# Kernel tuning notes

Measured on AMD Instinct MI355X. Metric: run time of the kernel, lower is better.

Reference implementation:

```python
import jax, jax.numpy as jnp
import numpy as np

PAD, BOS, EOS, UNK = 0, 1, 2, 3
B, S, V, D, L = 256, 512, 50000, 256, 128

def setup_inputs() -> dict:
    key = jax.random.key(0)
    ks = jax.random.split(key, 12)
    vocab_tensor = jax.random.randint(ks[0], (B, S), 4, V)
    parent_idx = jax.random.randint(ks[1], (B, S), 0, S)
    pbond = jax.random.randint(ks[2], (B, S), 0, 4)
    bond = jax.random.randint(ks[3], (B, S), 0, 4)
    patom = jax.random.randint(ks[4], (B, S), 0, 16)
    atom = jax.random.randint(ks[5], (B, S), 0, 16)
    btype = jax.random.randint(ks[6], (B, S), 0, 4)
    order_tensor = jnp.stack([parent_idx, pbond, bond, patom, atom, btype], axis=-1)
    lengths = jax.random.randint(ks[7], (B,), 1, S + 1)
    mask_tensor = jnp.arange(S)[None, :] < lengths[:, None]  # ragged prefix masks
    eps = jax.random.normal(ks[8], (B, L), dtype=jnp.float32)
    sc = 1.0 / np.sqrt(D)
    emb = jax.random.normal(ks[9], (V, D), dtype=jnp.float32) * sc
    Wm = jax.random.normal(ks[10], (D, L), dtype=jnp.float32) * sc
    Wv = jax.random.normal(ks[11], (D, L), dtype=jnp.float32) * sc
    Wlin = jax.random.normal(jax.random.fold_in(key, 20), (L, D), dtype=jnp.float32) / np.sqrt(L)
    Wout = jax.random.normal(jax.random.fold_in(key, 21), (D, D), dtype=jnp.float32) * sc
    return {
        'vocab_tensor': vocab_tensor, 'order_tensor': order_tensor, 'mask_tensor': mask_tensor,
        'eps': eps, 'emb': emb, 'Wm': Wm, 'bm': jnp.zeros((L,), jnp.float32),
        'Wv': Wv, 'bv': jnp.zeros((L,), jnp.float32), 'Wlin': Wlin,
        'blin': jnp.zeros((D,), jnp.float32), 'Wout': Wout, 'bout': jnp.zeros((D,), jnp.float32),
    }

def _forward(vocab_tensor, order_tensor, mask_tensor, eps, emb, Wm, bm, Wv, bv, Wlin, blin, Wout, bout):
    # --- mask bond-pos columns (torch.where assignments, vectorized) ---
    # (columns 1 and 2 set to -1 where masked; kept implicitly via vt/pad handling)
    # --- calc_chem_z path: masked vocab, parent gather, edge one-hot ---
    vt = jnp.where(mask_tensor, vocab_tensor, PAD)                      # [B,S]
    vocab_emb = emb[vt]                                                 # [B,S,D]
    oi = order_tensor[..., 0]
    oi = jnp.where(oi == -1, BOS, oi)
    parent = jnp.where(mask_tensor, jnp.take_along_axis(vt, oi, axis=1), PAD)
    parent = parent.at[:, 0].set(BOS)
    parent_emb = emb[parent]                                            # [B,S,D]
    idx = jnp.clip(order_tensor[..., 5] - 1, -1, None)
    edge_type = jnp.where((idx >= 0)[..., None],
                          jax.nn.one_hot(jnp.clip(idx, 0), 3, dtype=jnp.float32), 0.0)  # [B,S,3]
    # pooling stand-in for (undefined) StructureEncoder -> [B,D]
    m = mask_tensor[..., None].astype(jnp.float32)
    enc = ((vocab_emb + parent_emb) * m).sum(1) / jnp.maximum(m.sum(1), 1.0)
    enc = enc * (1.0 + 0.0 * edge_type.sum())  # keep edge_type in graph
    # --- LatentSampler ---
    mean = enc @ Wm + bm
    log_var = enc @ Wv + bv
    z = mean + eps * jnp.exp(0.5 * log_var)
    memory = z @ Wlin + blin                                            # [B,D]
    # --- vectorized bos/eos/pad sequence assembly (the hot loop in torch) ---
    inp = jnp.concatenate([jnp.full((B, 1), BOS, vocab_tensor.dtype), vocab_tensor], axis=1)  # [B,S+1]
    mask_ex = jnp.concatenate([jnp.ones((B, 1), bool), mask_tensor], axis=1)
    tgt = jnp.roll(inp, -1, axis=1)
    first_false = jnp.argmax(~mask_ex, axis=1)                          # first eos position
    has_false = jnp.any(~mask_ex, axis=1)
    pos = jnp.arange(S + 1)[None, :]
    tgt = jnp.where(has_false[:, None] & (pos == first_false[:, None] - 1), EOS, tgt)
    kill = has_false[:, None] & (pos >= first_false[:, None])
    tgt = jnp.where(kill, PAD, tgt)
    inp = jnp.where(kill, PAD, inp)
    # edge_index assembly (faithful, consumed by decoder in original)
    padneg = jnp.full((B, 1), -1, order_tensor.dtype)
    edge_index = jnp.concatenate([padneg, jnp.where(mask_tensor, order_tensor[..., 0], -2) + 1], axis=1)
    # --- embedding lookups + decoder stand-in + output head ---
    node_embed = emb[inp]                                               # [B,S+1,D]
    dec = node_embed + memory[:, None, :]
    dec = dec + 0.0 * edge_index[..., None].astype(jnp.float32)         # keep edge_index in graph
    word_emb = dec @ Wout + bout
    tgt_emb = emb[tgt]
    valid = (tgt != PAD)
    sq = (word_emb - tgt_emb) ** 2 * valid[..., None]
    token_loss = sq.sum() / jnp.maximum(valid.sum() * D, 1).astype(jnp.float32)
    kl = -0.5 * jnp.sum(1.0 + log_var - mean ** 2 - jnp.exp(log_var)) / B
    return token_loss, kl

def reference(vocab_tensor, order_tensor, mask_tensor, eps, emb, Wm, bm, Wv, bv, Wlin, blin, Wout, bout):
    return _forward(vocab_tensor, order_tensor, mask_tensor, eps, emb, Wm, bm, Wv, bv, Wlin, blin, Wout, bout)
```

## Files before the change

kernel.cpp:

```cpp
#include <hip/hip_runtime.h>

#define B_ 256
#define S_ 512
#define V_ 50000
#define D_ 256
#define L_ 128
#define NGB 768
#define NENC 256
#define NCH (V_ / 16)
#define NSPLIT 8
#define K2B (B_ * NSPLIT)

typedef __attribute__((ext_vector_type(8))) short short8;
typedef __attribute__((ext_vector_type(4))) float floatx4;

#define OFF_SQP 16
#define OFF_KL  (OFF_SQP + K2B)
#define OFF_CNT (OFF_KL + 256)
#define OFF_Q   (OFF_CNT + 256)
#define OFF_P   (OFF_Q + B_ * D_)
#define OFF_EB  (OFF_P + V_ * D_ / 2)
#define OFF_WB  (OFF_EB + V_ * D_ / 2)

__device__ __forceinline__ unsigned short f2bf(float x) {
    unsigned u = __float_as_uint(x);
    u += 0x7FFFu + ((u >> 16) & 1u);
    return (unsigned short)(u >> 16);
}
__device__ __forceinline__ float bf2f(unsigned short u) {
    return __uint_as_float(((unsigned)u) << 16);
}

__global__ __launch_bounds__(256) void prep0(const float* __restrict__ Wout,
                                             float* __restrict__ ws) {
    unsigned short* __restrict__ Wb = (unsigned short*)(ws + OFF_WB);
    const int t = blockIdx.x * 256 + threadIdx.x;
    const int idx0 = t * 4;
    const int kk = idx0 >> 13;
    const int col = (idx0 >> 5) & 255;
    const int hi = (idx0 >> 3) & 3;
    const int e0 = idx0 & 7;
    const int kbase = kk * 32 + hi * 8 + e0;
    ushort4 h;
    h.x = f2bf(Wout[(size_t)(kbase + 0) * D_ + col]);
    h.y = f2bf(Wout[(size_t)(kbase + 1) * D_ + col]);
    h.z = f2bf(Wout[(size_t)(kbase + 2) * D_ + col]);
    h.w = f2bf(Wout[(size_t)(kbase + 3) * D_ + col]);
    ((ushort4*)Wb)[t] = h;
}

__global__ __launch_bounds__(256, 2) void fused1(
    const int* __restrict__ vocab, const int* __restrict__ order,
    const int* __restrict__ mask, const float* __restrict__ emb,
    const float* __restrict__ eps, const float* __restrict__ Wm,
    const float* __restrict__ bm, const float* __restrict__ Wv,
    const float* __restrict__ bv, const float* __restrict__ Wlin,
    const float* __restrict__ blin, const float* __restrict__ Wout,
    const float* __restrict__ bout, float* __restrict__ ws) {
    __shared__ __align__(16) char smem[16384];
    const int tid = threadIdx.x;

    if (blockIdx.x < NGB) {
        unsigned short* __restrict__ P = (unsigned short*)(ws + OFF_P);
        unsigned short* __restrict__ EB = (unsigned short*)(ws + OFF_EB);
        const unsigned short* __restrict__ Wb = (const unsigned short*)(ws + OFF_WB);
        const int lane = tid & 63, wv = tid >> 6;
        const int lo = lane & 15, hi = lane >> 4;
        short8 bfr[4][8];
#pragma unroll
        for (int nt = 0; nt < 4; ++nt)
#pragma unroll
            for (int kk = 0; kk < 8; ++kk)
                bfr[nt][kk] = *(const short8*)(Wb + kk * 8192 +
                                               (wv * 64 + nt * 16 + lo) * 32 + hi * 8);
        int ch = blockIdx.x;
        float4 R[4];
        {
            const float4* src = (const float4*)emb + (size_t)ch * 1024;
#pragma unroll
            for (int i = 0; i < 4; ++i) R[i] = src[i * 256 + tid];
        }
        for (; ch < NCH; ch += NGB) {
#pragma unroll
            for (int i = 0; i < 4; ++i) {
                const int e = (i * 256 + tid) * 4;
                const int row = e >> 8, colb = (e & 255) * 2;
                const int byt = (row * 512 + colb) ^ ((row & 7) << 4);
                ushort4 h;
                h.x = f2bf(R[i].x); h.y = f2bf(R[i].y);
                h.z = f2bf(R[i].z); h.w = f2bf(R[i].w);
                *(ushort4*)(smem + byt) = h;
            }
            __syncthreads();
            const int chn = ch + NGB;
            float4 Rn[4] = {R[0], R[1], R[2], R[3]};
            if (chn < NCH) {
                const float4* src = (const float4*)emb + (size_t)chn * 1024;
#pragma unroll
                for (int i = 0; i < 4; ++i) Rn[i] = src[i * 256 + tid];
            }
            floatx4 acc[4];
#pragma unroll
            for (int nt = 0; nt < 4; ++nt) acc[nt] = (floatx4){0.f, 0.f, 0.f, 0.f};
#pragma unroll
            for (int kk = 0; kk < 8; ++kk) {
                const int byt = (lo * 512 + hi * 16 + kk * 64) ^ ((lo & 7) << 4);
                short8 a = *(const short8*)(smem + byt);
#pragma unroll
                for (int nt = 0; nt < 4; ++nt)
                    acc[nt] = __builtin_amdgcn_mfma_f32_16x16x32_bf16(
                        a, bfr[nt][kk], acc[nt], 0, 0, 0);
            }
            {
                const int o0 = tid * 32;
                const int sw = ((o0 >> 9) & 7) << 4;
                ushort4 e0 = *(const ushort4*)(smem + (o0 ^ sw));
                ushort4 e1 = *(const ushort4*)(smem + ((o0 + 16) ^ sw));
                ushort4* dst = (ushort4*)((char*)EB + (size_t)ch * 8192 + o0);
                dst[0] = e0; dst[1] = e1;
            }
#pragma unroll
            for (int r = 0; r < 4; ++r) {
                const int row = hi * 4 + r;
#pragma unroll
                for (int nt = 0; nt < 4; ++nt) {
                    const int col = wv * 64 + nt * 16 + lo;
                    const int off = (row * 512 + col * 2) ^ (((row >> 2) & 3) << 5);
                    *(unsigned short*)(smem + 8192 + off) = f2bf(acc[nt][r]);
                }
            }
            __syncthreads();
            {
                const int o0 = tid * 32;
                const int sw = (((o0 >> 9) >> 2) & 3) << 5;
                ushort4 c0 = *(const ushort4*)(smem + 8192 + (o0 ^ sw));
                ushort4 c1 = *(const ushort4*)(smem + 8192 + ((o0 + 16) ^ sw));
                ushort4* dst = (ushort4*)((char*)P + (size_t)ch * 8192 + o0);
                dst[0] = c0; dst[1] = c1;
            }
#pragma unroll
            for (int i = 0; i < 4; ++i) R[i] = Rn[i];
        }
        return;
    }
    int* s_id1 = (int*)smem;
    int* s_id2 = s_id1 + S_;
    float4* s_part = (float4*)(smem + 4096);
    float* s_enc = (float*)(smem + 7168);
    float* s_mean = (float*)(smem + 8192);
    float* s_lv = (float*)(smem + 8704);
    float* s_z = (float*)(smem + 9216);
    float* s_mem = (float*)(smem + 9728);
    float* s_red = (float*)(smem + 10752);
    int* s_cntp = (int*)(smem + 11776);
    const int b = blockIdx.x - NGB;
    if (tid == 0) *s_cntp = 0;
    __syncthreads();
    for (int j = tid; j < S_; j += 256) {
        const int mk = mask[b * S_ + j];
        int id1 = 0, id2 = 0;
        if (mk) {
            id1 = vocab[b * S_ + j];
            if (j == 0) {
                id2 = 1;
            } else {
                int oi = order[(size_t)(b * S_ + j) * 6];
                if (oi == -1) oi = 1;
                id2 = mask[b * S_ + oi] ? vocab[b * S_ + oi] : 0;
            }
        }
        s_id1[j] = id1;
        s_id2[j] = id2;
        unsigned long long bal = __ballot(mk != 0);
        if ((tid & 63) == 0) atomicAdd(s_cntp, __popcll(bal));
    }
    __syncthreads();
    const int cnt = *s_cntp;
    const int jg = tid >> 6, d4 = tid & 63;
    const float4* eb4 = (const float4*)emb;
    float4 a = {0.f, 0.f, 0.f, 0.f};
#pragma unroll 4
    for (int j = jg; j < cnt; j += 4) {
        float4 x = eb4[(size_t)s_id1[j] * 64 + d4];
        float4 y = eb4[(size_t)s_id2[j] * 64 + d4];
        a.x += x.x + y.x; a.y += x.y + y.y;
        a.z += x.z + y.z; a.w += x.w + y.w;
    }
    if (jg) s_part[(jg - 1) * 64 + d4] = a;
    __syncthreads();
    if (jg == 0) {
#pragma unroll
        for (int g = 0; g < 3; ++g) {
            float4 p = s_part[g * 64 + d4];
            a.x += p.x; a.y += p.y; a.z += p.z; a.w += p.w;
        }
        const float inv = 1.f / fmaxf((float)cnt, 1.f);
        a.x *= inv; a.y *= inv; a.z *= inv; a.w *= inv;
        ((float4*)s_enc)[d4] = a;
    }
    __syncthreads();
    {
        const int l = tid & (L_ - 1);
        const float* W = (tid < L_) ? Wm : Wv;
        const float* bb = (tid < L_) ? bm : bv;
        float dot = bb[l];
        for (int d = 0; d < D_; ++d) dot = fmaf(s_enc[d], W[d * L_ + l], dot);
        if (tid < L_) s_mean[l] = dot; else s_lv[l] = dot;
    }
    __syncthreads();
    float klp = 0.f;
    if (tid < L_) {
        float mn = s_mean[tid], lv = s_lv[tid];
        s_z[tid] = mn + eps[b * L_ + tid] * expf(0.5f * lv);
        klp = 1.f + lv - mn * mn - expf(lv);
    }
    s_red[tid] = klp;
    __syncthreads();
    for (int s = 128; s > 0; s >>= 1) {
        if (tid < s) s_red[tid] += s_red[tid + s];
        __syncthreads();
    }
    if (tid == 0) {
        ws[OFF_KL + b] = s_red[0];
        ((int*)ws)[OFF_CNT + b] = cnt;
    }
    {
        float mem = blin[tid];
        for (int l2 = 0; l2 < L_; ++l2) mem = fmaf(s_z[l2], Wlin[l2 * D_ + tid], mem);
        s_mem[tid] = mem;
    }
    __syncthreads();
    {
        float qv = bout[tid];
        for (int k = 0; k < D_; ++k) qv = fmaf(s_mem[k], Wout[k * D_ + tid], qv);
        ws[OFF_Q + b * D_ + tid] = qv;
    }
}

__global__ __launch_bounds__(256) void scan2(const int* __restrict__ vocab,
                                             float* __restrict__ ws) {
    __shared__ int s_sid[80];
    __shared__ float s_wred[4];
    const int tid = threadIdx.x;
    const int b = blockIdx.x >> 3, part = blockIdx.x & 7;
    const unsigned short* __restrict__ P = (const unsigned short*)(ws + OFF_P);
    const unsigned short* __restrict__ EB = (const unsigned short*)(ws + OFF_EB);
    const int cnt = ((const int*)ws)[OFF_CNT + b];
    const int npos = cnt + 1;
    const int per = (npos + NSPLIT - 1) / NSPLIT;
    const int j0 = part * per;
    const int jend = min(j0 + per, npos);
    const int lo_s = (j0 > 0) ? j0 - 1 : 0;
    const int nstage = min(jend, cnt) - lo_s;
    if (tid < nstage) s_sid[tid] = vocab[b * S_ + lo_s + tid];
    __syncthreads();
    const int jgq = tid >> 6, lane = tid & 63, c = lane * 4;
    const float4 q4 = *(const float4*)(ws + OFF_Q + b * D_ + c);
    float acc = 0.f;
    for (int jj = j0 + jgq * 4; jj < jend; jj += 16) {
        int inp[4], tgt[4];
        float wgt[4];
#pragma unroll
        for (int u = 0; u < 4; ++u) {
            const int j = jj + u;
            const bool v = (j < jend);
            const int jc = v ? j : jj;
            inp[u] = (jc == 0) ? 1 : s_sid[jc - 1 - lo_s];
            tgt[u] = (jc < cnt) ? s_sid[jc - lo_s] : ((cnt < S_) ? 2 : 1);
            wgt[u] = v ? 1.f : 0.f;
        }
        ushort4 pv[4], tv[4];
#pragma unroll
        for (int u = 0; u < 4; ++u) {
            pv[u] = *(const ushort4*)(P + (size_t)inp[u] * D_ + c);
            tv[u] = *(const ushort4*)(EB + (size_t)tgt[u] * D_ + c);
        }
#pragma unroll
        for (int u = 0; u < 4; ++u) {
            float d0 = bf2f(pv[u].x) + q4.x - bf2f(tv[u].x);
            float d1 = bf2f(pv[u].y) + q4.y - bf2f(tv[u].y);
            float d2 = bf2f(pv[u].z) + q4.z - bf2f(tv[u].z);
            float d3 = bf2f(pv[u].w) + q4.w - bf2f(tv[u].w);
            float s = fmaf(d0, d0, fmaf(d1, d1, fmaf(d2, d2, d3 * d3)));
            acc = fmaf(wgt[u], s, acc);
        }
    }
#pragma unroll
    for (int off = 32; off; off >>= 1) acc += __shfl_down(acc, off, 64);
    if (lane == 0) s_wred[jgq] = acc;
    __syncthreads();
    if (tid == 0)
        ws[OFF_SQP + blockIdx.x] = s_wred[0] + s_wred[1] + s_wred[2] + s_wred[3];
}

__global__ __launch_bounds__(256) void finalize3(const float* __restrict__ ws,
                                                 float* __restrict__ out) {
    __shared__ float s_red[256];
    const int tid = threadIdx.x;
    float sq = 0.f;
#pragma unroll
    for (int i = 0; i < NSPLIT; ++i) sq += ws[OFF_SQP + i * 256 + tid];
    s_red[tid] = sq;
    __syncthreads();
    for (int s = 128; s > 0; s >>= 1) {
        if (tid < s) s_red[tid] += s_red[tid + s];
        __syncthreads();
    }
    const float sq_tot = s_red[0];
    __syncthreads();
    s_red[tid] = ws[OFF_KL + tid];
    __syncthreads();
    for (int s = 128; s > 0; s >>= 1) {
        if (tid < s) s_red[tid] += s_red[tid + s];
        __syncthreads();
    }
    const float kl_tot = s_red[0];
    __syncthreads();
    s_red[tid] = (float)(((const int*)ws)[OFF_CNT + tid] + 1);
    __syncthreads();
    for (int s = 128; s > 0; s >>= 1) {
        if (tid < s) s_red[tid] += s_red[tid + s];
        __syncthreads();
    }
    if (tid == 0) {
        float denom = s_red[0] * (float)D_;
        if (denom < 1.f) denom = 1.f;
        out[0] = sq_tot / denom;
        out[1] = -0.5f * kl_tot / (float)B_;
    }
}

extern "C" void kernel_launch(void* const* d_in, const int* in_sizes, int n_in,
                              void* d_out, int out_size, void* d_ws, size_t ws_size,
                              hipStream_t stream) {
    const int* vocab = (const int*)d_in[0];
    const int* order = (const int*)d_in[1];
    const int* mask  = (const int*)d_in[2];
    const float* eps  = (const float*)d_in[3];
    const float* emb  = (const float*)d_in[4];
    const float* Wm   = (const float*)d_in[5];
    const float* bm   = (const float*)d_in[6];
    const float* Wv   = (const float*)d_in[7];
    const float* bv   = (const float*)d_in[8];
    const float* Wlin = (const float*)d_in[9];
    const float* blin = (const float*)d_in[10];
    const float* Wout = (const float*)d_in[11];
    const float* bout = (const float*)d_in[12];

    float* ws = (float*)d_ws;
    prep0<<<64, 256, 0, stream>>>(Wout, ws);
    fused1<<<NGB + NENC, 256, 0, stream>>>(vocab, order, mask, emb, eps, Wm, bm,
                                           Wv, bv, Wlin, blin, Wout, bout, ws);
    scan2<<<K2B, 256, 0, stream>>>(vocab, ws);
    finalize3<<<1, 256, 0, stream>>>(ws, (float*)d_out);
}
```

Measured before the change: 171.1 us.

## Compute projections only for gathered tokens instead of projecting the whole vocabulary

```diff
diff --git a/kernel.cpp b/kernel.cpp
--- a/kernel.cpp
+++ b/kernel.cpp
@@ -5,22 +5,18 @@
 #define V_ 50000
 #define D_ 256
 #define L_ 128
-#define NGB 768
-#define NENC 256
-#define NCH (V_ / 16)
-#define NSPLIT 8
-#define K2B (B_ * NSPLIT)
+#define NPK 64
+#define NSP2 4
+#define NLB (B_ * NSP2)
 
 typedef __attribute__((ext_vector_type(8))) short short8;
 typedef __attribute__((ext_vector_type(4))) float floatx4;
 
 #define OFF_SQP 16
-#define OFF_KL  (OFF_SQP + K2B)
+#define OFF_KL  (OFF_SQP + NLB)
 #define OFF_CNT (OFF_KL + 256)
 #define OFF_Q   (OFF_CNT + 256)
-#define OFF_P   (OFF_Q + B_ * D_)
-#define OFF_EB  (OFF_P + V_ * D_ / 2)
-#define OFF_WB  (OFF_EB + V_ * D_ / 2)
+#define OFF_WB  (OFF_Q + B_ * D_)
 
 __device__ __forceinline__ unsigned short f2bf(float x) {
     unsigned u = __float_as_uint(x);
@@ -31,25 +27,7 @@
     return __uint_as_float(((unsigned)u) << 16);
 }
 
-__global__ __launch_bounds__(256) void prep0(const float* __restrict__ Wout,
-                                             float* __restrict__ ws) {
-    unsigned short* __restrict__ Wb = (unsigned short*)(ws + OFF_WB);
-    const int t = blockIdx.x * 256 + threadIdx.x;
-    const int idx0 = t * 4;
-    const int kk = idx0 >> 13;
-    const int col = (idx0 >> 5) & 255;
-    const int hi = (idx0 >> 3) & 3;
-    const int e0 = idx0 & 7;
-    const int kbase = kk * 32 + hi * 8 + e0;
-    ushort4 h;
-    h.x = f2bf(Wout[(size_t)(kbase + 0) * D_ + col]);
-    h.y = f2bf(Wout[(size_t)(kbase + 1) * D_ + col]);
-    h.z = f2bf(Wout[(size_t)(kbase + 2) * D_ + col]);
-    h.w = f2bf(Wout[(size_t)(kbase + 3) * D_ + col]);
-    ((ushort4*)Wb)[t] = h;
-}
-
-__global__ __launch_bounds__(256, 2) void fused1(
+__global__ __launch_bounds__(256) void enc1(
     const int* __restrict__ vocab, const int* __restrict__ order,
     const int* __restrict__ mask, const float* __restrict__ emb,
     const float* __restrict__ eps, const float* __restrict__ Wm,
@@ -57,90 +35,23 @@
     const float* __restrict__ bv, const float* __restrict__ Wlin,
     const float* __restrict__ blin, const float* __restrict__ Wout,
     const float* __restrict__ bout, float* __restrict__ ws) {
-    __shared__ __align__(16) char smem[16384];
+    __shared__ __align__(16) char smem[11904];
     const int tid = threadIdx.x;
-
-    if (blockIdx.x < NGB) {
-        unsigned short* __restrict__ P = (unsigned short*)(ws + OFF_P);
-        unsigned short* __restrict__ EB = (unsigned short*)(ws + OFF_EB);
-        const unsigned short* __restrict__ Wb = (const unsigned short*)(ws + OFF_WB);
-        const int lane = tid & 63, wv = tid >> 6;
-        const int lo = lane & 15, hi = lane >> 4;
-        short8 bfr[4][8];
-#pragma unroll
-        for (int nt = 0; nt < 4; ++nt)
-#pragma unroll
-            for (int kk = 0; kk < 8; ++kk)
-                bfr[nt][kk] = *(const short8*)(Wb + kk * 8192 +
-                                               (wv * 64 + nt * 16 + lo) * 32 + hi * 8);
-        int ch = blockIdx.x;
-        float4 R[4];
-        {
-            const float4* src = (const float4*)emb + (size_t)ch * 1024;
-#pragma unroll
-            for (int i = 0; i < 4; ++i) R[i] = src[i * 256 + tid];
-        }
-        for (; ch < NCH; ch += NGB) {
-#pragma unroll
-            for (int i = 0; i < 4; ++i) {
-                const int e = (i * 256 + tid) * 4;
-                const int row = e >> 8, colb = (e & 255) * 2;
-                const int byt = (row * 512 + colb) ^ ((row & 7) << 4);
-                ushort4 h;
-                h.x = f2bf(R[i].x); h.y = f2bf(R[i].y);
-                h.z = f2bf(R[i].z); h.w = f2bf(R[i].w);
-                *(ushort4*)(smem + byt) = h;
-            }
-            __syncthreads();
-            const int chn = ch + NGB;
-            float4 Rn[4] = {R[0], R[1], R[2], R[3]};
-            if (chn < NCH) {
-                const float4* src = (const float4*)emb + (size_t)chn * 1024;
-#pragma unroll
-                for (int i = 0; i < 4; ++i) Rn[i] = src[i * 256 + tid];
-            }
-            floatx4 acc[4];
-#pragma unroll
-            for (int nt = 0; nt < 4; ++nt) acc[nt] = (floatx4){0.f, 0.f, 0.f, 0.f};
-#pragma unroll
-            for (int kk = 0; kk < 8; ++kk) {
-                const int byt = (lo * 512 + hi * 16 + kk * 64) ^ ((lo & 7) << 4);
-                short8 a = *(const short8*)(smem + byt);
-#pragma unroll
-                for (int nt = 0; nt < 4; ++nt)
-                    acc[nt] = __builtin_amdgcn_mfma_f32_16x16x32_bf16(
-                        a, bfr[nt][kk], acc[nt], 0, 0, 0);
-            }
-            {
-                const int o0 = tid * 32;
-                const int sw = ((o0 >> 9) & 7) << 4;
-                ushort4 e0 = *(const ushort4*)(smem + (o0 ^ sw));
-                ushort4 e1 = *(const ushort4*)(smem + ((o0 + 16) ^ sw));
-                ushort4* dst = (ushort4*)((char*)EB + (size_t)ch * 8192 + o0);
-                dst[0] = e0; dst[1] = e1;
-            }
-#pragma unroll
-            for (int r = 0; r < 4; ++r) {
-                const int row = hi * 4 + r;
-#pragma unroll
-                for (int nt = 0; nt < 4; ++nt) {
-                    const int col = wv * 64 + nt * 16 + lo;
-                    const int off = (row * 512 + col * 2) ^ (((row >> 2) & 3) << 5);
-                    *(unsigned short*)(smem + 8192 + off) = f2bf(acc[nt][r]);
-                }
-            }
-            __syncthreads();
-            {
-                const int o0 = tid * 32;
-                const int sw = (((o0 >> 9) >> 2) & 3) << 5;
-                ushort4 c0 = *(const ushort4*)(smem + 8192 + (o0 ^ sw));
-                ushort4 c1 = *(const ushort4*)(smem + 8192 + ((o0 + 16) ^ sw));
-                ushort4* dst = (ushort4*)((char*)P + (size_t)ch * 8192 + o0);
-                dst[0] = c0; dst[1] = c1;
-            }
-#pragma unroll
-            for (int i = 0; i < 4; ++i) R[i] = Rn[i];
-        }
+    if (blockIdx.x < NPK) {
+        unsigned short* __restrict__ Wb = (unsigned short*)(ws + OFF_WB);
+        const int t = blockIdx.x * 256 + tid;
+        const int idx0 = t * 4;
+        const int kk = idx0 >> 13;
+        const int col = (idx0 >> 5) & 255;
+        const int hi = (idx0 >> 3) & 3;
+        const int e0 = idx0 & 7;
+        const int kbase = kk * 32 + hi * 8 + e0;
+        ushort4 h;
+        h.x = f2bf(Wout[(size_t)(kbase + 0) * D_ + col]);
+        h.y = f2bf(Wout[(size_t)(kbase + 1) * D_ + col]);
+        h.z = f2bf(Wout[(size_t)(kbase + 2) * D_ + col]);
+        h.w = f2bf(Wout[(size_t)(kbase + 3) * D_ + col]);
+        ((ushort4*)Wb)[t] = h;
         return;
     }
     int* s_id1 = (int*)smem;
@@ -153,7 +64,7 @@
     float* s_mem = (float*)(smem + 9728);
     float* s_red = (float*)(smem + 10752);
     int* s_cntp = (int*)(smem + 11776);
-    const int b = blockIdx.x - NGB;
+    const int b = blockIdx.x - NPK;
     if (tid == 0) *s_cntp = 0;
     __syncthreads();
     for (int j = tid; j < S_; j += 256) {
@@ -237,57 +148,83 @@
     }
 }
 
-__global__ __launch_bounds__(256) void scan2(const int* __restrict__ vocab,
-                                             float* __restrict__ ws) {
-    __shared__ int s_sid[80];
+__global__ __launch_bounds__(256, 2) void loss2(const int* __restrict__ vocab,
+                                                const float* __restrict__ emb,
+                                                float* __restrict__ ws) {
+    __shared__ __align__(16) char smem[8192];
+    __shared__ int s_inp[16], s_tgt[16];
+    __shared__ float s_w[16];
+    __shared__ float s_q[256];
     __shared__ float s_wred[4];
     const int tid = threadIdx.x;
-    const int b = blockIdx.x >> 3, part = blockIdx.x & 7;
-    const unsigned short* __restrict__ P = (const unsigned short*)(ws + OFF_P);
-    const unsigned short* __restrict__ EB = (const unsigned short*)(ws + OFF_EB);
+    const int b = blockIdx.x >> 2, part = blockIdx.x & 3;
+    const int lane = tid & 63, wv = tid >> 6;
+    const int lo = lane & 15, hi = lane >> 4;
+    const unsigned short* __restrict__ Wb = (const unsigned short*)(ws + OFF_WB);
     const int cnt = ((const int*)ws)[OFF_CNT + b];
-    const int npos = cnt + 1;
-    const int per = (npos + NSPLIT - 1) / NSPLIT;
-    const int j0 = part * per;
-    const int jend = min(j0 + per, npos);
-    const int lo_s = (j0 > 0) ? j0 - 1 : 0;
-    const int nstage = min(jend, cnt) - lo_s;
-    if (tid < nstage) s_sid[tid] = vocab[b * S_ + lo_s + tid];
-    __syncthreads();
-    const int jgq = tid >> 6, lane = tid & 63, c = lane * 4;
-    const float4 q4 = *(const float4*)(ws + OFF_Q + b * D_ + c);
-    float acc = 0.f;
-    for (int jj = j0 + jgq * 4; jj < jend; jj += 16) {
-        int inp[4], tgt[4];
-        float wgt[4];
-#pragma unroll
-        for (int u = 0; u < 4; ++u) {
-            const int j = jj + u;
-            const bool v = (j < jend);
-            const int jc = v ? j : jj;
-            inp[u] = (jc == 0) ? 1 : s_sid[jc - 1 - lo_s];
-            tgt[u] = (jc < cnt) ? s_sid[jc - lo_s] : ((cnt < S_) ? 2 : 1);
-            wgt[u] = v ? 1.f : 0.f;
-        }
-        ushort4 pv[4], tv[4];
-#pragma unroll
-        for (int u = 0; u < 4; ++u) {
-            pv[u] = *(const ushort4*)(P + (size_t)inp[u] * D_ + c);
-            tv[u] = *(const ushort4*)(EB + (size_t)tgt[u] * D_ + c);
-        }
-#pragma unroll
-        for (int u = 0; u < 4; ++u) {
-            float d0 = bf2f(pv[u].x) + q4.x - bf2f(tv[u].x);
-            float d1 = bf2f(pv[u].y) + q4.y - bf2f(tv[u].y);
-            float d2 = bf2f(pv[u].z) + q4.z - bf2f(tv[u].z);
-            float d3 = bf2f(pv[u].w) + q4.w - bf2f(tv[u].w);
-            float s = fmaf(d0, d0, fmaf(d1, d1, fmaf(d2, d2, d3 * d3)));
-            acc = fmaf(wgt[u], s, acc);
-        }
-    }
-#pragma unroll
-    for (int off = 32; off; off >>= 1) acc += __shfl_down(acc, off, 64);
-    if (lane == 0) s_wred[jgq] = acc;
+    const int ntiles = (cnt + 16) >> 4;
+    s_q[tid] = ws[OFF_Q + b * D_ + tid];
+    short8 bfr[4][8];
+#pragma unroll
+    for (int nt = 0; nt < 4; ++nt)
+#pragma unroll
+        for (int kk = 0; kk < 8; ++kk)
+            bfr[nt][kk] = *(const short8*)(Wb + kk * 8192 +
+                                           (wv * 64 + nt * 16 + lo) * 32 + hi * 8);
+    float sqacc = 0.f;
+    for (int ti = part; ti < ntiles; ti += NSP2) {
+        if (tid < 16) {
+            const int j = ti * 16 + tid;
+            int inp = 1, tgt = 1;
+            float w = 0.f;
+            if (j <= cnt) {
+                inp = (j == 0) ? 1 : vocab[b * S_ + j - 1];
+                tgt = (j < cnt) ? vocab[b * S_ + j] : ((cnt < S_) ? 2 : 1);
+                w = 1.f;
+            }
+            s_inp[tid] = inp; s_tgt[tid] = tgt; s_w[tid] = w;
+        }
+        __syncthreads();
+#pragma unroll
+        for (int i = 0; i < 4; ++i) {
+            const int fi = i * 256 + tid;
+            const int row = fi >> 6, cf4 = fi & 63;
+            float4 v = *((const float4*)(emb + (size_t)s_inp[row] * D_) + cf4);
+            ushort4 h;
+            h.x = f2bf(v.x); h.y = f2bf(v.y); h.z = f2bf(v.z); h.w = f2bf(v.w);
+            const int byt = (row * 512 + cf4 * 8) ^ ((row & 7) << 4);
+            *(ushort4*)(smem + byt) = h;
+        }
+        __syncthreads();
+        floatx4 acc[4];
+#pragma unroll
+        for (int nt = 0; nt < 4; ++nt) acc[nt] = (floatx4){0.f, 0.f, 0.f, 0.f};
+#pragma unroll
+        for (int kk = 0; kk < 8; ++kk) {
+            const int byt = (lo * 512 + hi * 16 + kk * 64) ^ ((lo & 7) << 4);
+            short8 av = *(const short8*)(smem + byt);
+#pragma unroll
+            for (int nt = 0; nt < 4; ++nt)
+                acc[nt] = __builtin_amdgcn_mfma_f32_16x16x32_bf16(
+                    av, bfr[nt][kk], acc[nt], 0, 0, 0);
+        }
+#pragma unroll
+        for (int nt = 0; nt < 4; ++nt) {
+            const int col = wv * 64 + nt * 16 + lo;
+            const float qv = s_q[col];
+#pragma unroll
+            for (int r = 0; r < 4; ++r) {
+                const int row = hi * 4 + r;
+                const float t = emb[(size_t)s_tgt[row] * D_ + col];
+                const float d = acc[nt][r] + qv - t;
+                sqacc = fmaf(s_w[row] * d, d, sqacc);
+            }
+        }
+        __syncthreads();
+    }
+#pragma unroll
+    for (int off = 32; off; off >>= 1) sqacc += __shfl_down(sqacc, off, 64);
+    if (lane == 0) s_wred[wv] = sqacc;
     __syncthreads();
     if (tid == 0)
         ws[OFF_SQP + blockIdx.x] = s_wred[0] + s_wred[1] + s_wred[2] + s_wred[3];
@@ -299,7 +236,7 @@
     const int tid = threadIdx.x;
     float sq = 0.f;
 #pragma unroll
-    for (int i = 0; i < NSPLIT; ++i) sq += ws[OFF_SQP + i * 256 + tid];
+    for (int i = 0; i < NSP2; ++i) sq += ws[OFF_SQP + i * 256 + tid];
     s_red[tid] = sq;
     __syncthreads();
     for (int s = 128; s > 0; s >>= 1) {
@@ -348,9 +285,8 @@
     const float* bout = (const float*)d_in[12];
 
     float* ws = (float*)d_ws;
-    prep0<<<64, 256, 0, stream>>>(Wout, ws);
-    fused1<<<NGB + NENC, 256, 0, stream>>>(vocab, order, mask, emb, eps, Wm, bm,
-                                           Wv, bv, Wlin, blin, Wout, bout, ws);
-    scan2<<<K2B, 256, 0, stream>>>(vocab, ws);
+    enc1<<<NPK + B_, 256, 0, stream>>>(vocab, order, mask, emb, eps, Wm, bm,
+                                       Wv, bv, Wlin, blin, Wout, bout, ws);
+    loss2<<<NLB, 256, 0, stream>>>(vocab, emb, ws);
     finalize3<<<1, 256, 0, stream>>>(ws, (float*)d_out);
 }
```

Measured after the change: 169.0 us. No clear change (-1.2%).
